# Performance work log

Hardware: AMD Instinct MI355X
Metric: run time of the kernel (lower is better)

The kernel has to match this reference:

```python
import jax, jax.numpy as jnp
import numpy as np
import math

B, T, H, N2 = 4, 64, 1280, 32  # batch, seq, d_model, d_state//2
D_IN = 224 * 224 * 3
R_HID, N_CLS = 64, 60


def setup_inputs() -> dict:
    key = jax.random.key(0)
    ks = jax.random.split(key, 12)
    x = jax.random.normal(ks[0], (B, T, 224, 224, 3), jnp.float32)
    # bottleneck Linear(D_IN, H)
    Wb = jax.random.normal(ks[1], (H, D_IN), jnp.float32) / math.sqrt(D_IN)
    bb = jnp.zeros((H,), jnp.float32)
    # S4D kernel params (is_real=True path)
    log_dt_min, log_dt_max = math.log(1e-3), math.log(1e-1)
    log_dt = jax.random.uniform(ks[2], (H,), jnp.float32, log_dt_min, log_dt_max)
    C = jax.random.normal(ks[3], (H, N2), jnp.float32)
    log_A_real = jnp.log(0.5 * jnp.ones((H, N2), jnp.float32))
    D = jax.random.normal(ks[4], (H,), jnp.float32)
    # output_linear: Conv1d(H, 2H, 1) + GLU(dim=-2)
    Wc = jax.random.normal(ks[5], (2 * H, H), jnp.float32) / math.sqrt(H)
    bc = jnp.zeros((2 * H,), jnp.float32)
    # readout MLP
    W1 = jax.random.normal(ks[6], (R_HID, H), jnp.float32) / math.sqrt(H)
    b1 = jnp.zeros((R_HID,), jnp.float32)
    W2 = jax.random.normal(ks[7], (N_CLS, R_HID), jnp.float32) / math.sqrt(R_HID)
    b2 = jnp.zeros((N_CLS,), jnp.float32)
    return {"x": x, "Wb": Wb, "bb": bb, "log_dt": log_dt, "C": C,
            "log_A_real": log_A_real, "D": D, "Wc": Wc, "bc": bc,
            "W1": W1, "b1": b1, "W2": W2, "b2": b2}


def _s4d_kernel(log_dt, log_A_real, C, L):
    # is_real=True: A real negative diagonal, C real. K: (H, L)
    dt = jnp.exp(log_dt)                      # (H,)
    A = -jnp.exp(log_A_real)                  # (H, N2)
    dtA = A * dt[:, None]                     # (H, N2)
    Cb = C * (jnp.exp(dtA) - 1.0) / A         # (H, N2)
    vand = jnp.exp(dtA[:, :, None] * jnp.arange(L, dtype=dtA.dtype))  # (H, N2, L)
    return 2.0 * jnp.einsum("hn,hnl->hl", Cb, vand)


def reference(x, Wb, bb, log_dt, C, log_A_real, D, Wc, bc, W1, b1, W2, b2):
    b, t = x.shape[0], x.shape[1]
    xf = x.reshape(b, t, -1)                  # (B, T, D_IN)
    u = xf @ Wb.T + bb                        # (B, T, H) bottleneck
    ut = jnp.swapaxes(u, -1, -2)              # (B, H, L) transposed=False path
    L = t
    k = _s4d_kernel(log_dt, log_A_real, C, L)  # (H, L)
    # FFT convolution (length 2L, causal crop)
    k_f = jnp.fft.rfft(k, n=2 * L)            # (H, L+1)
    u_f = jnp.fft.rfft(ut, n=2 * L)           # (B, H, L+1)
    y = jnp.fft.irfft(u_f * k_f, n=2 * L)[..., :L]
    y = y + ut * D[:, None]                   # skip connection
    y = jax.nn.gelu(y, approximate=False)     # torch GELU (exact)
    # 1x1 conv to 2H then GLU along channel dim
    z = jnp.einsum("oh,bhl->bol", Wc, y) + bc[None, :, None]
    a, g = jnp.split(z, 2, axis=1)
    y = a * jax.nn.sigmoid(g)                 # (B, H, L)
    y = jnp.swapaxes(y, -1, -2)               # (B, L, H)
    last = y[:, -1, :]                        # (B, H)
    h = jax.nn.relu(last @ W1.T + b1)
    return h @ W2.T + b2                      # (B, N_CLS)
```

## Files before the change

kernel.cpp:

```cpp
#include <hip/hip_runtime.h>
#include <hip/hip_bf16.h>
#include <math.h>

typedef __attribute__((ext_vector_type(8))) short short8;
typedef __attribute__((ext_vector_type(4))) float f32x4;
typedef __attribute__((ext_vector_type(4))) unsigned int u32x4;

#define KDIM 150528
#define KDIMB ((long)KDIM * 4)
#define NT_TILES 10
#define KCHUNKS 24
#define STEPS 196
#define BK 32
#define HDIM 1280
#define MDIM 256
#define PSTRIDE (MDIM * HDIM)
#define ABYTES 32768
#define BUFB 49152

__device__ __forceinline__ unsigned int pk2(float a, float b) {
  unsigned int r;
  asm("v_cvt_pk_bf16_f32 %0, %1, %2" : "=v"(r) : "v"(a), "v"(b));
  return r;
}

__device__ __forceinline__ void gload16(const void* g, const char* l) {
  __builtin_amdgcn_global_load_lds(
      (const __attribute__((address_space(1))) unsigned int*)g,
      (__attribute__((address_space(3))) unsigned int*)l, 16, 0, 0);
}

__device__ __forceinline__ short8 cvt8(f32x4 lo, f32x4 hi) {
  union { u32x4 u; short8 s; } c;
  c.u = (u32x4){pk2(lo.x, lo.y), pk2(lo.z, lo.w), pk2(hi.x, hi.y), pk2(hi.z, hi.w)};
  return c.s;
}

__global__ __launch_bounds__(512, 2) void k_gemm(
    const float* __restrict__ X, const float* __restrict__ W,
    float* __restrict__ P) {
  extern __shared__ char smem[];
  const int swz = (blockIdx.x & 7) * 30 + (blockIdx.x >> 3);
  const int kc = swz / 10;
  const int nt = swz % 10;
  const long k0b = (long)kc * (BK * STEPS) * 4;

  const int tid = threadIdx.x;
  const int lane = tid & 63;
  const int wv = tid >> 6;
  const int wm = wv >> 1, wn = wv & 1;
  const int frow = lane & 15;
  const int cbase = (lane >> 4) << 5;

  const int srow = tid >> 3;
  const int perm = ((tid & 7) ^ (srow & 7)) << 4;
  const char* xbase = (const char*)X + (long)srow * KDIMB + k0b + perm;
  const char* wbase = (const char*)W + (long)(nt * 128 + srow) * KDIMB + k0b + perm;

  int aoffl[4], aoffh[4], boffl[4], boffh[4];
#pragma unroll
  for (int i = 0; i < 4; ++i) {
    const int Ra = wm * 64 + i * 16 + frow;
    const int swa = (Ra & 7) << 4;
    aoffl[i] = Ra * 128 + (cbase ^ swa);
    aoffh[i] = Ra * 128 + ((cbase + 16) ^ swa);
    const int Rb = wn * 64 + i * 16 + frow;
    const int swb = (Rb & 7) << 4;
    boffl[i] = ABYTES + Rb * 128 + (cbase ^ swb);
    boffh[i] = ABYTES + Rb * 128 + ((cbase + 16) ^ swb);
  }

  f32x4 acc[4][4];
#pragma unroll
  for (int i = 0; i < 4; ++i)
#pragma unroll
    for (int j = 0; j < 4; ++j) acc[i][j] = (f32x4){0.f, 0.f, 0.f, 0.f};

#define STAGE(buf, t)                                                         \
  {                                                                           \
    const long ko = (long)(t) * (BK * 4);                                     \
    _Pragma("unroll") for (int q = 0; q < 4; ++q)                             \
        gload16(xbase + (long)q * 64 * KDIMB + ko,                            \
                (buf) + q * 8192 + wv * 1024);                                \
    _Pragma("unroll") for (int q = 0; q < 2; ++q)                             \
        gload16(wbase + (long)q * 64 * KDIMB + ko,                            \
                (buf) + ABYTES + q * 8192 + wv * 1024);                       \
  }

#define LOADFRAGS(buf)                                                        \
  f32x4 a0l = *(const f32x4*)((buf) + aoffl[0]),                              \
        a0h = *(const f32x4*)((buf) + aoffh[0]),                              \
        a1l = *(const f32x4*)((buf) + aoffl[1]),                              \
        a1h = *(const f32x4*)((buf) + aoffh[1]),                              \
        a2l = *(const f32x4*)((buf) + aoffl[2]),                              \
        a2h = *(const f32x4*)((buf) + aoffh[2]),                              \
        a3l = *(const f32x4*)((buf) + aoffl[3]),                              \
        a3h = *(const f32x4*)((buf) + aoffh[3]),                              \
        b0l = *(const f32x4*)((buf) + boffl[0]),                              \
        b0h = *(const f32x4*)((buf) + boffh[0]),                              \
        b1l = *(const f32x4*)((buf) + boffl[1]),                              \
        b1h = *(const f32x4*)((buf) + boffh[1]),                              \
        b2l = *(const f32x4*)((buf) + boffl[2]),                              \
        b2h = *(const f32x4*)((buf) + boffh[2]),                              \
        b3l = *(const f32x4*)((buf) + boffl[3]),                              \
        b3h = *(const f32x4*)((buf) + boffh[3]);

#define CVTMFMA()                                                             \
  {                                                                           \
    short8 fa[4], fb[4];                                                      \
    fa[0] = cvt8(a0l, a0h); fa[1] = cvt8(a1l, a1h);                           \
    fa[2] = cvt8(a2l, a2h); fa[3] = cvt8(a3l, a3h);                           \
    fb[0] = cvt8(b0l, b0h); fb[1] = cvt8(b1l, b1h);                           \
    fb[2] = cvt8(b2l, b2h); fb[3] = cvt8(b3l, b3h);                           \
    _Pragma("unroll") for (int i = 0; i < 4; ++i)                             \
        _Pragma("unroll") for (int j = 0; j < 4; ++j)                         \
            acc[i][j] = __builtin_amdgcn_mfma_f32_16x16x32_bf16(              \
                fa[i], fb[j], acc[i][j], 0, 0, 0);                            \
  }

  char* b_cur = smem;
  char* b_nxt = smem + BUFB;
  char* b_stg = smem + 2 * BUFB;

  STAGE(b_cur, 0);
  STAGE(b_nxt, 1);

  for (int t = 0; t < STEPS - 1; ++t) {
    asm volatile("s_waitcnt vmcnt(6)" ::: "memory");
    __builtin_amdgcn_s_barrier();
    __builtin_amdgcn_sched_barrier(0);
    LOADFRAGS(b_cur);
    __builtin_amdgcn_sched_barrier(0);
    if (t + 2 < STEPS) STAGE(b_stg, t + 2);
    __builtin_amdgcn_sched_barrier(0);
    __builtin_amdgcn_s_setprio(1);
    CVTMFMA();
    __builtin_amdgcn_s_setprio(0);
    char* tmp = b_cur; b_cur = b_nxt; b_nxt = b_stg; b_stg = tmp;
  }
  asm volatile("s_waitcnt vmcnt(0)" ::: "memory");
  __builtin_amdgcn_s_barrier();
  __builtin_amdgcn_sched_barrier(0);
  {
    LOADFRAGS(b_cur);
    CVTMFMA();
  }

#undef STAGE
#undef LOADFRAGS
#undef CVTMFMA

  float* Pc = P + (long)kc * PSTRIDE + nt * 128;
  const int rb = wm * 64 + ((lane >> 4) << 2);
  const int cb = wn * 64 + frow;
#pragma unroll
  for (int i = 0; i < 4; ++i)
#pragma unroll
    for (int j = 0; j < 4; ++j) {
      const int col = cb + j * 16;
#pragma unroll
      for (int r = 0; r < 4; ++r)
        Pc[(long)(rb + i * 16 + r) * HDIM + col] = acc[i][j][r];
    }
}

__global__ __launch_bounds__(256) void k_s4d(
    const float* __restrict__ log_dt, const float* __restrict__ lar,
    const float* __restrict__ C, float* __restrict__ ktab) {
  const int idx = blockIdx.x * 256 + threadIdx.x;
  const int h = idx >> 6, l = idx & 63;
  const float dt = expf(log_dt[h]);
  const float fl = (float)l;
  float acc = 0.f;
#pragma unroll 4
  for (int n = 0; n < 32; ++n) {
    const float A = -expf(lar[h * 32 + n]);
    const float dtA = A * dt;
    const float Cb = C[h * 32 + n] * expm1f(dtA) / A;
    acc += Cb * expf(dtA * fl);
  }
  ktab[idx] = 2.f * acc;
}

__global__ __launch_bounds__(256) void k_red(
    const float* __restrict__ P, const float* __restrict__ bb,
    float* __restrict__ U) {
  const int idx = blockIdx.x * 256 + threadIdx.x;
  float s = bb[idx % HDIM];
#pragma unroll
  for (int c = 0; c < KCHUNKS; ++c) s += P[(long)c * PSTRIDE + idx];
  U[idx] = s;
}

__global__ __launch_bounds__(256) void k_conv(
    const float* __restrict__ U, const float* __restrict__ ktab,
    const float* __restrict__ Dv, float* __restrict__ y63) {
  __shared__ float kt[64 * 65];
  const int t = threadIdx.x;
  const int hw = blockIdx.x * 64;
  for (int i = t; i < 4096; i += 256)
    kt[(i >> 6) * 65 + (i & 63)] = ktab[(hw + (i >> 6)) * 64 + (i & 63)];
  __syncthreads();
  const int hl = t & 63, b = t >> 6;
  const int h = hw + hl;
  float y = 0.f;
  for (int m = 0; m < 64; ++m)
    y += U[(long)(b * 64 + m) * HDIM + h] * kt[hl * 65 + (63 - m)];
  y += Dv[h] * U[(long)(b * 64 + 63) * HDIM + h];
  y63[b * HDIM + h] = 0.5f * y * (1.f + erff(y * 0.70710678118654752f));
}

__global__ __launch_bounds__(64) void k_gate(
    const float* __restrict__ y63, const float* __restrict__ Wc,
    const float* __restrict__ bc, float* __restrict__ lastv) {
  const int r = blockIdx.x;
  const int l = threadIdx.x;
  const float* wa = Wc + (long)r * HDIM;
  const float* wg = Wc + (long)(HDIM + r) * HDIM;
  float sa[4] = {0.f, 0.f, 0.f, 0.f}, sg[4] = {0.f, 0.f, 0.f, 0.f};
#pragma unroll
  for (int seg = 0; seg < 5; ++seg) {
    const int j = seg * 256 + l * 4;
    const f32x4 a4 = *(const f32x4*)(wa + j);
    const f32x4 g4 = *(const f32x4*)(wg + j);
#pragma unroll
    for (int b = 0; b < 4; ++b) {
      const f32x4 yv = *(const f32x4*)(y63 + b * HDIM + j);
      sa[b] += a4.x * yv.x + a4.y * yv.y + a4.z * yv.z + a4.w * yv.w;
      sg[b] += g4.x * yv.x + g4.y * yv.y + g4.z * yv.z + g4.w * yv.w;
    }
  }
#pragma unroll
  for (int off = 32; off; off >>= 1)
#pragma unroll
    for (int b = 0; b < 4; ++b) {
      sa[b] += __shfl_down(sa[b], off);
      sg[b] += __shfl_down(sg[b], off);
    }
  if (l == 0) {
    const float ba = bc[r], bg = bc[HDIM + r];
#pragma unroll
    for (int b = 0; b < 4; ++b) {
      const float za = ba + sa[b], zg = bg + sg[b];
      lastv[b * HDIM + r] = za / (1.f + expf(-zg));
    }
  }
}

__global__ __launch_bounds__(64) void k_head(
    const float* __restrict__ lastv, const float* __restrict__ W1,
    const float* __restrict__ b1, const float* __restrict__ W2,
    const float* __restrict__ b2, float* __restrict__ out) {
  __shared__ float ll[HDIM];
  __shared__ float h1[64];
  const int b = blockIdx.x, t = threadIdx.x;
  for (int i = t; i < HDIM; i += 64) ll[i] = lastv[b * HDIM + i];
  __syncthreads();
  {
    const float* w = W1 + t * HDIM;
    float s = b1[t];
    for (int j = 0; j < HDIM; j += 4) {
      const f32x4 wv = *(const f32x4*)(w + j);
      s += wv.x * ll[j] + wv.y * ll[j + 1] + wv.z * ll[j + 2] + wv.w * ll[j + 3];
    }
    h1[t] = fmaxf(s, 0.f);
  }
  __syncthreads();
  if (t < 60) {
    const float* w = W2 + t * 64;
    float o = b2[t];
#pragma unroll
    for (int r = 0; r < 64; ++r) o += w[r] * h1[r];
    out[b * 60 + t] = o;
  }
}

extern "C" void kernel_launch(void* const* d_in, const int* in_sizes, int n_in,
                              void* d_out, int out_size, void* d_ws, size_t ws_size,
                              hipStream_t stream) {
  const float* x   = (const float*)d_in[0];
  const float* Wb  = (const float*)d_in[1];
  const float* bb  = (const float*)d_in[2];
  const float* ldt = (const float*)d_in[3];
  const float* C   = (const float*)d_in[4];
  const float* lar = (const float*)d_in[5];
  const float* Dv  = (const float*)d_in[6];
  const float* Wc  = (const float*)d_in[7];
  const float* bc  = (const float*)d_in[8];
  const float* W1  = (const float*)d_in[9];
  const float* b1  = (const float*)d_in[10];
  const float* W2  = (const float*)d_in[11];
  const float* b2  = (const float*)d_in[12];
  float* out = (float*)d_out;

  float* P     = (float*)d_ws;
  float* ktab  = P + (long)KCHUNKS * PSTRIDE;
  float* U     = ktab + HDIM * 64;
  float* y63   = U + PSTRIDE;
  float* lastv = y63 + 4 * HDIM;

  (void)hipFuncSetAttribute(reinterpret_cast<const void*>(k_gemm),
                            hipFuncAttributeMaxDynamicSharedMemorySize,
                            3 * BUFB);

  k_s4d<<<320, 256, 0, stream>>>(ldt, lar, C, ktab);
  k_gemm<<<NT_TILES * KCHUNKS, 512, 3 * BUFB, stream>>>(x, Wb, P);
  k_red<<<PSTRIDE / 256, 256, 0, stream>>>(P, bb, U);
  k_conv<<<20, 256, 0, stream>>>(U, ktab, Dv, y63);
  k_gate<<<HDIM, 64, 0, stream>>>(y63, Wc, bc, lastv);
  k_head<<<4, 64, 0, stream>>>(lastv, W1, b1, W2, b2, out);
}
```

Baseline: 296.0 us.

## Split GEMM into 128x128 tiles with 256-thread blocks and double buffering

Changes the bottleneck GEMM from 256x128 output tiles computed by 512-thread blocks to 128x128 tiles computed by 256-thread blocks. This doubles the grid to 480 blocks, which spreads the work across more CUs. The three-buffer LDS ring is replaced by two buffers, with an extra barrier after the fragment reads so the current buffer can be overwritten by the next stage. The trade is that each X row tile is now fetched by twice as many blocks, so global traffic for x goes up, and every step pays an added sync.

```diff
diff --git a/kernel.cpp b/kernel.cpp
--- a/kernel.cpp
+++ b/kernel.cpp
@@ -9,14 +9,15 @@
 #define KDIM 150528
 #define KDIMB ((long)KDIM * 4)
 #define NT_TILES 10
+#define MT_TILES 2
 #define KCHUNKS 24
 #define STEPS 196
 #define BK 32
 #define HDIM 1280
 #define MDIM 256
 #define PSTRIDE (MDIM * HDIM)
-#define ABYTES 32768
-#define BUFB 49152
+#define ABYTES 16384
+#define BUFB 32768
 
 __device__ __forceinline__ unsigned int pk2(float a, float b) {
   unsigned int r;
@@ -36,13 +37,15 @@
   return c.s;
 }
 
-__global__ __launch_bounds__(512, 2) void k_gemm(
+__global__ __launch_bounds__(256, 2) void k_gemm(
     const float* __restrict__ X, const float* __restrict__ W,
     float* __restrict__ P) {
   extern __shared__ char smem[];
-  const int swz = (blockIdx.x & 7) * 30 + (blockIdx.x >> 3);
-  const int kc = swz / 10;
-  const int nt = swz % 10;
+  const int swz = (blockIdx.x & 7) * 60 + (blockIdx.x >> 3);
+  const int kc = swz / 20;
+  const int rem = swz % 20;
+  const int nt = rem >> 1;
+  const int mt = rem & 1;
   const long k0b = (long)kc * (BK * STEPS) * 4;
 
   const int tid = threadIdx.x;
@@ -54,7 +57,7 @@
 
   const int srow = tid >> 3;
   const int perm = ((tid & 7) ^ (srow & 7)) << 4;
-  const char* xbase = (const char*)X + (long)srow * KDIMB + k0b + perm;
+  const char* xbase = (const char*)X + (long)(mt * 128 + srow) * KDIMB + k0b + perm;
   const char* wbase = (const char*)W + (long)(nt * 128 + srow) * KDIMB + k0b + perm;
 
   int aoffl[4], aoffh[4], boffl[4], boffh[4];
@@ -80,11 +83,11 @@
   {                                                                           \
     const long ko = (long)(t) * (BK * 4);                                     \
     _Pragma("unroll") for (int q = 0; q < 4; ++q)                             \
-        gload16(xbase + (long)q * 64 * KDIMB + ko,                            \
-                (buf) + q * 8192 + wv * 1024);                                \
-    _Pragma("unroll") for (int q = 0; q < 2; ++q)                             \
-        gload16(wbase + (long)q * 64 * KDIMB + ko,                            \
-                (buf) + ABYTES + q * 8192 + wv * 1024);                       \
+        gload16(xbase + (long)q * 32 * KDIMB + ko,                            \
+                (buf) + q * 4096 + wv * 1024);                                \
+    _Pragma("unroll") for (int q = 0; q < 4; ++q)                             \
+        gload16(wbase + (long)q * 32 * KDIMB + ko,                            \
+                (buf) + ABYTES + q * 4096 + wv * 1024);                       \
   }
 
 #define LOADFRAGS(buf)                                                        \
@@ -118,31 +121,31 @@
                 fa[i], fb[j], acc[i][j], 0, 0, 0);                            \
   }
 
-  char* b_cur = smem;
-  char* b_nxt = smem + BUFB;
-  char* b_stg = smem + 2 * BUFB;
-
-  STAGE(b_cur, 0);
-  STAGE(b_nxt, 1);
+  STAGE(smem, 0);
+  STAGE(smem + BUFB, 1);
 
   for (int t = 0; t < STEPS - 1; ++t) {
-    asm volatile("s_waitcnt vmcnt(6)" ::: "memory");
+    char* cbuf = smem + (t & 1) * BUFB;
+    asm volatile("s_waitcnt vmcnt(8)" ::: "memory");
     __builtin_amdgcn_s_barrier();
     __builtin_amdgcn_sched_barrier(0);
-    LOADFRAGS(b_cur);
+    LOADFRAGS(cbuf);
+    asm volatile("s_waitcnt lgkmcnt(0)" ::: "memory");
     __builtin_amdgcn_sched_barrier(0);
-    if (t + 2 < STEPS) STAGE(b_stg, t + 2);
+    __builtin_amdgcn_s_barrier();
+    __builtin_amdgcn_sched_barrier(0);
+    if (t + 2 < STEPS) STAGE(cbuf, t + 2);
     __builtin_amdgcn_sched_barrier(0);
     __builtin_amdgcn_s_setprio(1);
     CVTMFMA();
     __builtin_amdgcn_s_setprio(0);
-    char* tmp = b_cur; b_cur = b_nxt; b_nxt = b_stg; b_stg = tmp;
   }
   asm volatile("s_waitcnt vmcnt(0)" ::: "memory");
   __builtin_amdgcn_s_barrier();
   __builtin_amdgcn_sched_barrier(0);
   {
-    LOADFRAGS(b_cur);
+    char* cbuf = smem + ((STEPS - 1) & 1) * BUFB;
+    LOADFRAGS(cbuf);
     CVTMFMA();
   }
 
@@ -150,7 +153,7 @@
 #undef LOADFRAGS
 #undef CVTMFMA
 
-  float* Pc = P + (long)kc * PSTRIDE + nt * 128;
+  float* Pc = P + (long)kc * PSTRIDE + (long)mt * 128 * HDIM + nt * 128;
   const int rb = wm * 64 + ((lane >> 4) << 2);
   const int cb = wn * 64 + frow;
 #pragma unroll
@@ -301,10 +304,10 @@
 
   (void)hipFuncSetAttribute(reinterpret_cast<const void*>(k_gemm),
                             hipFuncAttributeMaxDynamicSharedMemorySize,
-                            3 * BUFB);
+                            2 * BUFB);
 
   k_s4d<<<320, 256, 0, stream>>>(ldt, lar, C, ktab);
-  k_gemm<<<NT_TILES * KCHUNKS, 512, 3 * BUFB, stream>>>(x, Wb, P);
+  k_gemm<<<NT_TILES * MT_TILES * KCHUNKS, 256, 2 * BUFB, stream>>>(x, Wb, P);
   k_red<<<PSTRIDE / 256, 256, 0, stream>>>(P, bb, U);
   k_conv<<<20, 256, 0, stream>>>(U, ktab, Dv, y63);
   k_gate<<<HDIM, 64, 0, stream>>>(y63, Wc, bc, lastv);
```

Measured after the change: 343.2 us. 16.0% more time.
